# Kernel optimization log

Hardware: AMD Instinct MI355X
Metric: run time of the kernel (lower is better)

The kernel has to match this reference:

```python
import jax, jax.numpy as jnp
import numpy as np

B, N, D = 64, 256, 1024      # batch, n_patches (DINOv2 ViT-L/14 @224), feature dim
P, C = 2000, 200             # num_prototypes, num_classes (10 per class)
EPS = 1e-4


def setup_inputs() -> dict:
    key = jax.random.key(0)
    k1, k2 = jax.random.split(key)
    patches = jax.random.normal(k1, (B, N, D), dtype=jnp.float32)
    prototypes = jax.random.uniform(k2, (P, D), dtype=jnp.float32)  # torch.rand init
    # fc init: +1 for the prototype's own class, -0.5 elsewhere (_fc_init)
    per_class = P // C
    cls = jnp.arange(P) // per_class                     # [P]
    pos = jax.nn.one_hot(cls, C, dtype=jnp.float32)      # [P, C]
    fc_w = (1.0 * pos + (-0.5) * (1.0 - pos)).T          # [C, P]
    return {"patches": patches, "prototypes": prototypes, "fc_w": fc_w}


def reference(patches, prototypes, fc_w):
    x2 = jnp.sum(patches ** 2, axis=-1, keepdims=True)   # [B, N, 1] (== x2 @ ones.T broadcast)
    p2 = jnp.sum(prototypes ** 2, axis=-1)               # [P]
    xp = jnp.einsum('bnd,pd->bnp', patches, prototypes)  # [B, N, P]
    distances = jax.nn.relu(x2 - 2.0 * xp + p2[None, None, :])  # [B, N, P]
    # permute(0, 2, 1)
    attn_maps = jnp.transpose(distances, (0, 2, 1))       # [B, P, N]
    # -max_pool1d(-d, kernel=N) == min over patches
    min_distances = jnp.min(attn_maps, axis=-1)           # [B, P]
    # 'log' activation similarity
    prototype_activations = jnp.log((min_distances + 1.0) / (min_distances + EPS))
    logits = prototype_activations @ fc_w.T               # [B, C]
    return logits, attn_maps, min_distances
```

## Files before the change

kernel.cpp:

```cpp
#include <hip/hip_runtime.h>
#include <hip/hip_bf16.h>
#include <stdint.h>

#define B_   64
#define N_   256
#define D_   1024
#define P_   2000
#define C_   200
#define PP   2048
#define M_   (B_ * N_)
#define EPSA 1e-4f

#define BM   256
#define BN   256
#define BK   64
#define NT   (D_ / BK)

using f32x4  = __attribute__((ext_vector_type(4))) float;
using bf16x8 = __attribute__((ext_vector_type(8))) short;

__device__ __forceinline__ unsigned short f2bf(float f) {
  uint32_t u = __builtin_bit_cast(uint32_t, f);
  uint32_t r = (u + 0x7FFFu + ((u >> 16) & 1u)) >> 16;
  return (unsigned short)r;
}

__global__ __launch_bounds__(256) void k_convert(
    const float* __restrict__ patches, const float* __restrict__ protos,
    unsigned short* __restrict__ pat_bf, unsigned short* __restrict__ pro_bf,
    float* __restrict__ x2, float* __restrict__ p2)
{
  const int row = blockIdx.x;
  const int t   = threadIdx.x;
  float4 v = make_float4(0.f, 0.f, 0.f, 0.f);
  if (row < M_) {
    v = *(const float4*)(patches + (size_t)row * D_ + t * 4);
  } else {
    const int p = row - M_;
    if (p < P_) v = *(const float4*)(protos + (size_t)p * D_ + t * 4);
  }
  ushort4 o;
  o.x = f2bf(v.x); o.y = f2bf(v.y); o.z = f2bf(v.z); o.w = f2bf(v.w);
  if (row < M_) *(ushort4*)(pat_bf + (size_t)row * D_ + t * 4) = o;
  else          *(ushort4*)(pro_bf + (size_t)(row - M_) * D_ + t * 4) = o;

  float s = v.x * v.x + v.y * v.y + v.z * v.z + v.w * v.w;
  #pragma unroll
  for (int off = 32; off >= 1; off >>= 1) s += __shfl_xor(s, off);
  __shared__ float sm[4];
  if ((t & 63) == 0) sm[t >> 6] = s;
  __syncthreads();
  if (t == 0) {
    const float tot = sm[0] + sm[1] + sm[2] + sm[3];
    if (row < M_) x2[row] = tot;
    else          p2[row - M_] = tot;
  }
}

#define VMW4 asm volatile("s_waitcnt vmcnt(4)" ::: "memory")
#define VMW2 asm volatile("s_waitcnt vmcnt(2)" ::: "memory")
#define VMW0 asm volatile("s_waitcnt vmcnt(0)" ::: "memory")
#define NOPW ((void)0)
#define BARR __builtin_amdgcn_s_barrier()

#define STAGE(KT, H, NB) do {                                                  \
  const int r0_ = ((H) >> 1) * 128;                                            \
  const unsigned short* gb_ = (((H) & 1) == 0)                                 \
      ? (pro_bf + (size_t)p0 * D_) : (pat_bf + (size_t)m0 * D_);               \
  unsigned short* lb_ = ((((H) & 1) == 0) ? ldsA : ldsB) + (NB) * (BM * BK);   \
  _Pragma("unroll")                                                            \
  for (int i_ = 0; i_ < 2; ++i_) {                                             \
    const int rr_  = r0_ + wid * 16 + i_ * 8;                                  \
    const int row_ = rr_ + (lane >> 3);                                        \
    const int sl_  = (lane & 7) ^ (row_ & 7);                                  \
    __builtin_amdgcn_global_load_lds(                                          \
      (const __attribute__((address_space(1))) void*)                          \
          (gb_ + (size_t)row_ * D_ + (KT) * BK + sl_ * 8),                     \
      (__attribute__((address_space(3))) void*)(lb_ + rr_ * BK), 16, 0, 0);    \
  }                                                                            \
} while (0)

#define PHASE(PH, NH, DOSTAGE, VMWAIT, DOBAR) do {                             \
  DOSTAGE;                                                                     \
  bf16x8 af_[4][2], bq_[2][2];                                                 \
  _Pragma("unroll")                                                            \
  for (int i_ = 0; i_ < 4; ++i_)                                               \
    _Pragma("unroll")                                                          \
    for (int kk_ = 0; kk_ < 2; ++kk_) {                                        \
      const int row_ = (PH) * 128 + wr * 64 + i_ * 16 + (lane & 15);           \
      const int sl_  = (kk_ * 4 + (lane >> 4)) ^ (row_ & 7);                   \
      af_[i_][kk_] = *(const bf16x8*)&ldsA[nb * (BM * BK) + row_ * BK + sl_ * 8];\
    }                                                                          \
  _Pragma("unroll")                                                            \
  for (int j_ = 0; j_ < 2; ++j_)                                               \
    _Pragma("unroll")                                                          \
    for (int kk_ = 0; kk_ < 2; ++kk_) {                                        \
      const int row_ = (NH) * 128 + wc * 32 + j_ * 16 + (lane & 15);           \
      const int sl_  = (kk_ * 4 + (lane >> 4)) ^ (row_ & 7);                   \
      bq_[j_][kk_] = *(const bf16x8*)&ldsB[nb * (BM * BK) + row_ * BK + sl_ * 8];\
    }                                                                          \
  __builtin_amdgcn_s_setprio(1);                                               \
  _Pragma("unroll")                                                            \
  for (int i_ = 0; i_ < 4; ++i_)                                               \
    _Pragma("unroll")                                                          \
    for (int j_ = 0; j_ < 2; ++j_)                                             \
      _Pragma("unroll")                                                        \
      for (int kk_ = 0; kk_ < 2; ++kk_)                                        \
        acc[(PH) * 4 + i_][(NH) * 2 + j_] =                                    \
            __builtin_amdgcn_mfma_f32_16x16x32_bf16(                           \
                af_[i_][kk_], bq_[j_][kk_],                                    \
                acc[(PH) * 4 + i_][(NH) * 2 + j_], 0, 0, 0);                   \
  __builtin_amdgcn_s_setprio(0);                                               \
  VMWAIT;                                                                      \
  __builtin_amdgcn_sched_barrier(0);                                           \
  DOBAR;                                                                       \
  __builtin_amdgcn_sched_barrier(0);                                           \
} while (0)

__global__ __launch_bounds__(512, 2) void k_gemm(
    const unsigned short* __restrict__ pro_bf,
    const unsigned short* __restrict__ pat_bf,
    const float* __restrict__ x2, const float* __restrict__ p2,
    float* __restrict__ attn, float* __restrict__ minv, float* __restrict__ act)
{
  extern __shared__ unsigned short lds_u16[];
  unsigned short* ldsA = lds_u16;
  unsigned short* ldsB = lds_u16 + 2 * BM * BK;
  float* wmin = (float*)lds_u16;

  const int tid  = threadIdx.x;
  const int lane = tid & 63;
  const int wid  = tid >> 6;
  const int wr   = wid >> 2;
  const int wc   = wid & 3;

  const int wg  = blockIdx.x;
  const int xcd = wg & 7;
  const int idx = wg >> 3;
  const int mt  = xcd * 8 + (idx & 7);
  const int pt  = idx >> 3;
  const int b   = mt;
  const int p0  = pt * BM;
  const int m0  = mt * BN;

  f32x4 acc[8][4];
  #pragma unroll
  for (int i = 0; i < 8; i++)
    #pragma unroll
    for (int j = 0; j < 4; j++) acc[i][j] = (f32x4){0.f, 0.f, 0.f, 0.f};

  STAGE(0, 0, 0); STAGE(0, 1, 0); STAGE(0, 2, 0); STAGE(0, 3, 0);
  VMW4;
  __builtin_amdgcn_sched_barrier(0);
  BARR;
  __builtin_amdgcn_sched_barrier(0);

  int nb = 0;
  #pragma unroll 1
  for (int kt = 0; kt < NT - 1; ++kt) {
    PHASE(0, 0, STAGE(kt + 1, 0, nb ^ 1), VMW4, BARR);
    PHASE(1, 0, STAGE(kt + 1, 1, nb ^ 1), VMW4, BARR);
    PHASE(1, 1, STAGE(kt + 1, 2, nb ^ 1), NOPW, BARR);
    PHASE(0, 1, STAGE(kt + 1, 3, nb ^ 1), VMW4, BARR);
    nb ^= 1;
  }
  PHASE(0, 0, NOPW, VMW2, BARR);
  PHASE(1, 0, NOPW, VMW0, BARR);
  PHASE(1, 1, NOPW, NOPW, NOPW);
  PHASE(0, 1, NOPW, NOPW, NOPW);

  __syncthreads();

  float x2v[2][2]; int nn[2][2];
  #pragma unroll
  for (int nh = 0; nh < 2; ++nh)
    #pragma unroll
    for (int j = 0; j < 2; ++j) {
      const int nl = nh * 128 + wc * 32 + j * 16 + (lane & 15);
      x2v[nh][j] = x2[m0 + nl];
      nn[nh][j]  = nl;
    }
  float* attn_b = attn + (size_t)b * (P_ * N_);

  #pragma unroll
  for (int pf = 0; pf < 8; ++pf) {
    #pragma unroll
    for (int q = 0; q < 4; ++q) {
      const int pl = (pf >> 2) * 128 + wr * 64 + (pf & 3) * 16 + (lane >> 4) * 4 + q;
      const int p  = p0 + pl;
      float mn = 3.4e38f;
      if (p < P_) {
        const float p2v = p2[p];
        float* rowp = attn_b + (size_t)p * N_;
        #pragma unroll
        for (int nh = 0; nh < 2; ++nh)
          #pragma unroll
          for (int j = 0; j < 2; ++j) {
            const float d = fmaxf(x2v[nh][j] + p2v - 2.0f * acc[pf][nh * 2 + j][q], 0.f);
            rowp[nn[nh][j]] = d;
            mn = fminf(mn, d);
          }
      }
      #pragma unroll
      for (int mask = 1; mask <= 8; mask <<= 1) mn = fminf(mn, __shfl_xor(mn, mask));
      if ((lane & 15) == 0) wmin[wc * 256 + pl] = mn;
    }
  }
  __syncthreads();
  if (tid < 256) {
    const int p = p0 + tid;
    if (p < P_) {
      const float m = fminf(fminf(wmin[tid], wmin[256 + tid]),
                            fminf(wmin[512 + tid], wmin[768 + tid]));
      minv[b * P_ + p] = m;
      act[b * P_ + p]  = logf((m + 1.0f) / (m + EPSA));
    }
  }
}

__global__ __launch_bounds__(256) void k_logits(
    const float* __restrict__ act, const float* __restrict__ fc_w,
    float* __restrict__ out)
{
  const int gw   = (blockIdx.x * 256 + threadIdx.x) >> 6;
  const int lane = threadIdx.x & 63;
  const int b = gw & 63;
  const int c = gw >> 6;
  const float* a = act  + (size_t)b * P_;
  const float* w = fc_w + (size_t)c * P_;
  float s = 0.f;
  #pragma unroll
  for (int i = 0; i < 32; i++) {
    const int p = i * 64 + lane;
    if (p < P_) s += a[p] * w[p];
  }
  #pragma unroll
  for (int off = 32; off >= 1; off >>= 1) s += __shfl_xor(s, off);
  if (lane == 0) out[b * C_ + c] = s;
}

#define GEMM_LDS_BYTES (4 * BM * BK * 2)

extern "C" void kernel_launch(void* const* d_in, const int* in_sizes, int n_in,
                              void* d_out, int out_size, void* d_ws, size_t ws_size,
                              hipStream_t stream)
{
  const float* patches = (const float*)d_in[0];
  const float* protos  = (const float*)d_in[1];
  const float* fc_w    = (const float*)d_in[2];

  float* out    = (float*)d_out;
  float* logits = out;
  float* attn   = out + (size_t)B_ * C_;
  float* minv   = out + (size_t)B_ * C_ + (size_t)B_ * P_ * N_;

  char* ws = (char*)d_ws;
  unsigned short* pat_bf = (unsigned short*)ws;  ws += (size_t)M_ * D_ * 2;
  unsigned short* pro_bf = (unsigned short*)ws;  ws += (size_t)PP * D_ * 2;
  float* x2  = (float*)ws;                       ws += (size_t)M_ * 4;
  float* p2  = (float*)ws;                       ws += (size_t)PP * 4;
  float* act = (float*)ws;

  (void)hipFuncSetAttribute((const void*)k_gemm,
                            hipFuncAttributeMaxDynamicSharedMemorySize,
                            GEMM_LDS_BYTES);

  hipLaunchKernelGGL(k_convert, dim3(M_ + PP), dim3(256), 0, stream,
                     patches, protos, pat_bf, pro_bf, x2, p2);
  hipLaunchKernelGGL(k_gemm, dim3((M_ / BN) * (PP / BM)), dim3(512),
                     GEMM_LDS_BYTES, stream,
                     pro_bf, pat_bf, x2, p2, attn, minv, act);
  hipLaunchKernelGGL(k_logits, dim3((B_ * C_) / 4), dim3(256), 0, stream,
                     act, fc_w, logits);
}
```

Baseline: 263.5 us.

## Restructure GEMM main loop by k-slice and use one wave per row in convert

The GEMM inner loop is reorganised so each phase covers one k-slice (kk) across all four B column fragments. B fragments are loaded once per half-iteration and reused across both A halves, which changes the staging order and the vmcnt waits. The convert kernel now handles four rows per block with one wavefront per row, removing the LDS reduction and __syncthreads. Together these aim to cut LDS reads and improve MFMA issue density, but the reordered stage/wait pattern must still keep data ready before each phase.

```diff
diff --git a/kernel.cpp b/kernel.cpp
--- a/kernel.cpp
+++ b/kernel.cpp
@@ -30,44 +30,42 @@
     unsigned short* __restrict__ pat_bf, unsigned short* __restrict__ pro_bf,
     float* __restrict__ x2, float* __restrict__ p2)
 {
-  const int row = blockIdx.x;
-  const int t   = threadIdx.x;
-  float4 v = make_float4(0.f, 0.f, 0.f, 0.f);
-  if (row < M_) {
-    v = *(const float4*)(patches + (size_t)row * D_ + t * 4);
-  } else {
-    const int p = row - M_;
-    if (p < P_) v = *(const float4*)(protos + (size_t)p * D_ + t * 4);
-  }
-  ushort4 o;
-  o.x = f2bf(v.x); o.y = f2bf(v.y); o.z = f2bf(v.z); o.w = f2bf(v.w);
-  if (row < M_) *(ushort4*)(pat_bf + (size_t)row * D_ + t * 4) = o;
-  else          *(ushort4*)(pro_bf + (size_t)(row - M_) * D_ + t * 4) = o;
-
-  float s = v.x * v.x + v.y * v.y + v.z * v.z + v.w * v.w;
+  const int row  = (blockIdx.x * 256 + threadIdx.x) >> 6;
+  const int lane = threadIdx.x & 63;
+  const bool pad = (row >= M_) && (row - M_ >= P_);
+  const float* src = (row < M_) ? patches + (size_t)row * D_
+                                : protos + (size_t)(row - M_) * D_;
+  unsigned short* dst = (row < M_) ? pat_bf + (size_t)row * D_
+                                   : pro_bf + (size_t)(row - M_) * D_;
+  float s = 0.f;
+  #pragma unroll
+  for (int k = 0; k < 4; ++k) {
+    float4 v = make_float4(0.f, 0.f, 0.f, 0.f);
+    if (!pad) v = ((const float4*)src)[lane + k * 64];
+    ushort4 o;
+    o.x = f2bf(v.x); o.y = f2bf(v.y); o.z = f2bf(v.z); o.w = f2bf(v.w);
+    ((ushort4*)dst)[lane + k * 64] = o;
+    s += v.x * v.x + v.y * v.y + v.z * v.z + v.w * v.w;
+  }
   #pragma unroll
   for (int off = 32; off >= 1; off >>= 1) s += __shfl_xor(s, off);
-  __shared__ float sm[4];
-  if ((t & 63) == 0) sm[t >> 6] = s;
-  __syncthreads();
-  if (t == 0) {
-    const float tot = sm[0] + sm[1] + sm[2] + sm[3];
-    if (row < M_) x2[row] = tot;
-    else          p2[row - M_] = tot;
-  }
-}
-
-#define VMW4 asm volatile("s_waitcnt vmcnt(4)" ::: "memory")
+  if (lane == 0) {
+    if (row < M_) x2[row] = s;
+    else          p2[row - M_] = s;
+  }
+}
+
 #define VMW2 asm volatile("s_waitcnt vmcnt(2)" ::: "memory")
 #define VMW0 asm volatile("s_waitcnt vmcnt(0)" ::: "memory")
 #define NOPW ((void)0)
 #define BARR __builtin_amdgcn_s_barrier()
 
 #define STAGE(KT, H, NB) do {                                                  \
-  const int r0_ = ((H) >> 1) * 128;                                            \
-  const unsigned short* gb_ = (((H) & 1) == 0)                                 \
+  const int isA_ = (((H) == 0) || ((H) == 3)) ? 1 : 0;                         \
+  const int r0_  = (((H) == 2) || ((H) == 3)) ? 128 : 0;                       \
+  const unsigned short* gb_ = isA_                                             \
       ? (pro_bf + (size_t)p0 * D_) : (pat_bf + (size_t)m0 * D_);               \
-  unsigned short* lb_ = ((((H) & 1) == 0) ? ldsA : ldsB) + (NB) * (BM * BK);   \
+  unsigned short* lb_ = (isA_ ? ldsA : ldsB) + (NB) * (BM * BK);               \
   _Pragma("unroll")                                                            \
   for (int i_ = 0; i_ < 2; ++i_) {                                             \
     const int rr_  = r0_ + wid * 16 + i_ * 8;                                  \
@@ -80,37 +78,36 @@
   }                                                                            \
 } while (0)
 
-#define PHASE(PH, NH, DOSTAGE, VMWAIT, DOBAR) do {                             \
-  DOSTAGE;                                                                     \
-  bf16x8 af_[4][2], bq_[2][2];                                                 \
+#define LOAD_B(KK) do {                                                        \
+  _Pragma("unroll")                                                            \
+  for (int j_ = 0; j_ < 4; ++j_) {                                             \
+    const int row_ = (j_ >> 1) * 128 + wc * 32 + (j_ & 1) * 16 + (lane & 15);  \
+    const int sl_  = ((KK) * 4 + (lane >> 4)) ^ (row_ & 7);                    \
+    bq[j_] = *(const bf16x8*)&ldsB[nb * (BM * BK) + row_ * BK + sl_ * 8];      \
+  }                                                                            \
+} while (0)
+
+#define LOAD_A(PH, KK) do {                                                    \
+  _Pragma("unroll")                                                            \
+  for (int i_ = 0; i_ < 4; ++i_) {                                             \
+    const int row_ = (PH) * 128 + wr * 64 + i_ * 16 + (lane & 15);             \
+    const int sl_  = ((KK) * 4 + (lane >> 4)) ^ (row_ & 7);                    \
+    af[i_] = *(const bf16x8*)&ldsA[nb * (BM * BK) + row_ * BK + sl_ * 8];      \
+  }                                                                            \
+} while (0)
+
+#define MFMA16(PH) do {                                                        \
+  __builtin_amdgcn_s_setprio(1);                                               \
   _Pragma("unroll")                                                            \
   for (int i_ = 0; i_ < 4; ++i_)                                               \
     _Pragma("unroll")                                                          \
-    for (int kk_ = 0; kk_ < 2; ++kk_) {                                        \
-      const int row_ = (PH) * 128 + wr * 64 + i_ * 16 + (lane & 15);           \
-      const int sl_  = (kk_ * 4 + (lane >> 4)) ^ (row_ & 7);                   \
-      af_[i_][kk_] = *(const bf16x8*)&ldsA[nb * (BM * BK) + row_ * BK + sl_ * 8];\
-    }                                                                          \
-  _Pragma("unroll")                                                            \
-  for (int j_ = 0; j_ < 2; ++j_)                                               \
-    _Pragma("unroll")                                                          \
-    for (int kk_ = 0; kk_ < 2; ++kk_) {                                        \
-      const int row_ = (NH) * 128 + wc * 32 + j_ * 16 + (lane & 15);           \
-      const int sl_  = (kk_ * 4 + (lane >> 4)) ^ (row_ & 7);                   \
-      bq_[j_][kk_] = *(const bf16x8*)&ldsB[nb * (BM * BK) + row_ * BK + sl_ * 8];\
-    }                                                                          \
-  __builtin_amdgcn_s_setprio(1);                                               \
-  _Pragma("unroll")                                                            \
-  for (int i_ = 0; i_ < 4; ++i_)                                               \
-    _Pragma("unroll")                                                          \
-    for (int j_ = 0; j_ < 2; ++j_)                                             \
-      _Pragma("unroll")                                                        \
-      for (int kk_ = 0; kk_ < 2; ++kk_)                                        \
-        acc[(PH) * 4 + i_][(NH) * 2 + j_] =                                    \
-            __builtin_amdgcn_mfma_f32_16x16x32_bf16(                           \
-                af_[i_][kk_], bq_[j_][kk_],                                    \
-                acc[(PH) * 4 + i_][(NH) * 2 + j_], 0, 0, 0);                   \
+    for (int j_ = 0; j_ < 4; ++j_)                                             \
+      acc[(PH) * 4 + i_][j_] = __builtin_amdgcn_mfma_f32_16x16x32_bf16(        \
+          af[i_], bq[j_], acc[(PH) * 4 + i_][j_], 0, 0, 0);                    \
   __builtin_amdgcn_s_setprio(0);                                               \
+} while (0)
+
+#define PH_END(VMWAIT, DOBAR) do {                                             \
   VMWAIT;                                                                      \
   __builtin_amdgcn_sched_barrier(0);                                           \
   DOBAR;                                                                       \
@@ -149,8 +146,11 @@
     #pragma unroll
     for (int j = 0; j < 4; j++) acc[i][j] = (f32x4){0.f, 0.f, 0.f, 0.f};
 
+  bf16x8 bq[4];
+  bf16x8 af[4];
+
   STAGE(0, 0, 0); STAGE(0, 1, 0); STAGE(0, 2, 0); STAGE(0, 3, 0);
-  VMW4;
+  VMW2;
   __builtin_amdgcn_sched_barrier(0);
   BARR;
   __builtin_amdgcn_sched_barrier(0);
@@ -158,28 +158,26 @@
   int nb = 0;
   #pragma unroll 1
   for (int kt = 0; kt < NT - 1; ++kt) {
-    PHASE(0, 0, STAGE(kt + 1, 0, nb ^ 1), VMW4, BARR);
-    PHASE(1, 0, STAGE(kt + 1, 1, nb ^ 1), VMW4, BARR);
-    PHASE(1, 1, STAGE(kt + 1, 2, nb ^ 1), NOPW, BARR);
-    PHASE(0, 1, STAGE(kt + 1, 3, nb ^ 1), VMW4, BARR);
+    STAGE(kt + 1, 0, nb ^ 1); LOAD_B(0); LOAD_A(0, 0); MFMA16(0); PH_END(VMW2, BARR);
+    STAGE(kt + 1, 1, nb ^ 1);            LOAD_A(1, 0); MFMA16(1); PH_END(NOPW, BARR);
+    STAGE(kt + 1, 2, nb ^ 1); LOAD_B(1); LOAD_A(0, 1); MFMA16(0); PH_END(NOPW, BARR);
+    STAGE(kt + 1, 3, nb ^ 1);            LOAD_A(1, 1); MFMA16(1); PH_END(VMW2, BARR);
     nb ^= 1;
   }
-  PHASE(0, 0, NOPW, VMW2, BARR);
-  PHASE(1, 0, NOPW, VMW0, BARR);
-  PHASE(1, 1, NOPW, NOPW, NOPW);
-  PHASE(0, 1, NOPW, NOPW, NOPW);
+  LOAD_B(0); LOAD_A(0, 0); MFMA16(0); PH_END(VMW0, BARR);
+             LOAD_A(1, 0); MFMA16(1); PH_END(NOPW, BARR);
+  LOAD_B(1); LOAD_A(0, 1); MFMA16(0); PH_END(NOPW, BARR);
+             LOAD_A(1, 1); MFMA16(1);
 
   __syncthreads();
 
-  float x2v[2][2]; int nn[2][2];
-  #pragma unroll
-  for (int nh = 0; nh < 2; ++nh)
-    #pragma unroll
-    for (int j = 0; j < 2; ++j) {
-      const int nl = nh * 128 + wc * 32 + j * 16 + (lane & 15);
-      x2v[nh][j] = x2[m0 + nl];
-      nn[nh][j]  = nl;
-    }
+  float x2v[4]; int nn[4];
+  #pragma unroll
+  for (int j = 0; j < 4; ++j) {
+    const int nl = (j >> 1) * 128 + wc * 32 + (j & 1) * 16 + (lane & 15);
+    x2v[j] = x2[m0 + nl];
+    nn[j]  = nl;
+  }
   float* attn_b = attn + (size_t)b * (P_ * N_);
 
   #pragma unroll
@@ -193,13 +191,11 @@
         const float p2v = p2[p];
         float* rowp = attn_b + (size_t)p * N_;
         #pragma unroll
-        for (int nh = 0; nh < 2; ++nh)
-          #pragma unroll
-          for (int j = 0; j < 2; ++j) {
-            const float d = fmaxf(x2v[nh][j] + p2v - 2.0f * acc[pf][nh * 2 + j][q], 0.f);
-            rowp[nn[nh][j]] = d;
-            mn = fminf(mn, d);
-          }
+        for (int j = 0; j < 4; ++j) {
+          const float d = fmaxf(x2v[j] + p2v - 2.0f * acc[pf][j][q], 0.f);
+          rowp[nn[j]] = d;
+          mn = fminf(mn, d);
+        }
       }
       #pragma unroll
       for (int mask = 1; mask <= 8; mask <<= 1) mn = fminf(mn, __shfl_xor(mn, mask));
@@ -265,7 +261,7 @@
                             hipFuncAttributeMaxDynamicSharedMemorySize,
                             GEMM_LDS_BYTES);
 
-  hipLaunchKernelGGL(k_convert, dim3(M_ + PP), dim3(256), 0, stream,
+  hipLaunchKernelGGL(k_convert, dim3((M_ + PP) / 4), dim3(256), 0, stream,
                      patches, protos, pat_bf, pro_bf, x2, p2);
   hipLaunchKernelGGL(k_gemm, dim3((M_ / BN) * (PP / BM)), dim3(512),
                      GEMM_LDS_BYTES, stream,
```

New measurement: 265.2 us. About the same (+0.6%).
